# Kernel tuning notes

Measured on AMD Instinct MI355X. Metric: run time of the kernel, lower is better.

Reference implementation:

```python
import jax, jax.numpy as jnp
import numpy as np

N_EMBED = 1024
EMBED_DIM = 64
DECAY = 0.99
EPS = 1e-05


def setup_inputs() -> dict:
    key = jax.random.key(0)
    k1, k2 = jax.random.split(key)
    z_e = jax.random.normal(k1, (16, 4096, EMBED_DIM), dtype=jnp.float32)
    # torch init: uniform_(-1/n_embed, 1/n_embed)
    embed = (jax.random.uniform(k2, (N_EMBED, EMBED_DIM), dtype=jnp.float32) * 2.0 - 1.0) / N_EMBED
    cluster_size = jnp.zeros((N_EMBED,), dtype=jnp.float32)
    embed_avg = embed.copy()
    return {"z_e": z_e, "embed": embed, "cluster_size": cluster_size, "embed_avg": embed_avg}


def reference(z_e, embed, cluster_size, embed_avg):
    B, N, E = z_e.shape
    flat = z_e.reshape(-1, E)  # [T, E], T = B*N
    dist = (jnp.sum(flat * flat, axis=1, keepdims=True)
            - 2.0 * flat @ embed.T
            + jnp.sum(embed * embed, axis=1)[None, :])  # [T, K]
    embed_ind = jnp.argmin(dist, axis=1)  # argmax(-dist)
    z_q = embed[embed_ind].reshape(B, N, E)

    # training-mode EMA statistics (scatter-add == one-hot matmul, but memory-efficient)
    onehot_sum = jnp.zeros((N_EMBED,), flat.dtype).at[embed_ind].add(1.0)
    embed_sum = jnp.zeros((N_EMBED, E), flat.dtype).at[embed_ind].add(flat)
    new_cluster_size = DECAY * cluster_size + (1.0 - DECAY) * onehot_sum
    new_embed_avg = DECAY * embed_avg + (1.0 - DECAY) * embed_sum
    n = jnp.sum(new_cluster_size)
    cs = (new_cluster_size + EPS) / (n + N_EMBED * EPS) * n
    new_embed = new_embed_avg / cs[:, None]

    diff = jnp.mean((jax.lax.stop_gradient(z_q) - z_e) ** 2)
    z_q_st = z_e + jax.lax.stop_gradient(z_q - z_e)  # straight-through
    return (z_q_st, diff, embed_ind.reshape(B, N), new_embed, new_cluster_size, new_embed_avg)
```

## Files before the change

### kernel.cpp

```cpp
#include <hip/hip_runtime.h>
#include <math.h>

#define T_TOK 65536
#define K_CODE 1024
#define E_DIM 64
#define DECAYF 0.99f
#define EPSF 1e-5f

#define TT 256
#define QCAP 4096
#define HACC 1.3e-3f

typedef short short8 __attribute__((ext_vector_type(8)));
typedef float f32x16 __attribute__((ext_vector_type(16)));

__device__ __forceinline__ float mul_nf(float a, float b) {
#pragma clang fp contract(off)
    return a * b;
}
__device__ __forceinline__ float add_nf(float a, float b) {
#pragma clang fp contract(off)
    return a + b;
}
__device__ __forceinline__ float sub_nf(float a, float b) {
#pragma clang fp contract(off)
    return a - b;
}

__device__ __forceinline__ float np_sq_row(const float* xrow) {
    const float4* xp = reinterpret_cast<const float4*>(xrow);
    float r[8];
#pragma unroll
    for (int g = 0; g < 8; ++g) {
        float4 va = xp[2 * g], vb = xp[2 * g + 1];
        float e[8] = {va.x, va.y, va.z, va.w, vb.x, vb.y, vb.z, vb.w};
#pragma unroll
        for (int j = 0; j < 8; ++j) {
            if (g == 0) r[j] = mul_nf(e[j], e[j]);
            else        r[j] = add_nf(r[j], mul_nf(e[j], e[j]));
        }
    }
    float s01 = add_nf(r[0], r[1]);
    float s23 = add_nf(r[2], r[3]);
    float s45 = add_nf(r[4], r[5]);
    float s67 = add_nf(r[6], r[7]);
    return add_nf(add_nf(s01, s23), add_nf(s45, s67));
}

__device__ __forceinline__ unsigned f2bf_rne(float f) {
    unsigned u = __float_as_uint(f);
    u += 0x7FFFu + ((u >> 16) & 1u);
    return (u >> 16);
}

__device__ __forceinline__ void exact_key(int t0, int tl, int code, float wn,
                                          const float* __restrict__ z_e,
                                          const float* __restrict__ embed,
                                          const float* xn_s,
                                          unsigned long long* key_s) {
    const float4* xp = reinterpret_cast<const float4*>(z_e + (size_t)(t0 + tl) * E_DIM);
    const float4* wp = reinterpret_cast<const float4*>(embed + (size_t)code * E_DIM);
    float d = 0.f;
#pragma unroll
    for (int m = 0; m < 16; ++m) {
        float4 x4 = xp[m];
        float4 w4 = wp[m];
        d = __builtin_fmaf(x4.x, w4.x, d);
        d = __builtin_fmaf(x4.y, w4.y, d);
        d = __builtin_fmaf(x4.z, w4.z, d);
        d = __builtin_fmaf(x4.w, w4.w, d);
    }
    float dist = add_nf(sub_nf(xn_s[tl], d + d), wn);
    unsigned b = __float_as_uint(dist);
    unsigned mk = (b & 0x80000000u) ? ~b : (b | 0x80000000u);
    atomicMin(key_s + tl, ((unsigned long long)mk << 32) | (unsigned)code);
}


__global__ __launch_bounds__(512) void dist_kernel(const float* __restrict__ z_e,
                                                   const float* __restrict__ embed,
                                                   float* __restrict__ out_zq,
                                                   float* __restrict__ out_ind,
                                                   float* __restrict__ diff_acc,
                                                   float* __restrict__ esum_rep,
                                                   float* __restrict__ onehot_rep,
                                                   int rep_mask) {
    __shared__ unsigned short Ws[K_CODE * E_DIM];
    __shared__ float wn_s[K_CODE];
    __shared__ float xn_s[TT];
    __shared__ unsigned long long key_s[TT];
    __shared__ unsigned q_s[QCAP];
    __shared__ int bi_s[TT];
    __shared__ int qc_s;

    int tid = threadIdx.x;
    int lane = tid & 63;
    int wave = tid >> 6;
    int g = lane >> 5;
    int t0 = blockIdx.x * TT;

    if (tid == 0) qc_s = 0;
    if (tid < TT) {
        key_s[tid] = ~0ull;
        xn_s[tid] = np_sq_row(z_e + (size_t)(t0 + tid) * E_DIM);
    }

#pragma unroll
    for (int rr = 0; rr < 2; ++rr) {
        int row = tid + rr * 512;
        const float4* wp = reinterpret_cast<const float4*>(embed + (size_t)row * E_DIM);
        uint4* WsQ = reinterpret_cast<uint4*>(Ws);
        float r8[8];
#pragma unroll
        for (int gq = 0; gq < 8; ++gq) {
            float4 va = wp[2 * gq], vb = wp[2 * gq + 1];
            float e[8] = {va.x, va.y, va.z, va.w, vb.x, vb.y, vb.z, vb.w};
#pragma unroll
            for (int j = 0; j < 8; ++j) {
                if (gq == 0) r8[j] = mul_nf(e[j], e[j]);
                else         r8[j] = add_nf(r8[j], mul_nf(e[j], e[j]));
            }
            unsigned p0 = f2bf_rne(e[0]) | (f2bf_rne(e[1]) << 16);
            unsigned p1 = f2bf_rne(e[2]) | (f2bf_rne(e[3]) << 16);
            unsigned p2 = f2bf_rne(e[4]) | (f2bf_rne(e[5]) << 16);
            unsigned p3 = f2bf_rne(e[6]) | (f2bf_rne(e[7]) << 16);
            WsQ[row * 8 + (gq ^ (row & 7))] = make_uint4(p0, p1, p2, p3);
        }
        float s01 = add_nf(r8[0], r8[1]);
        float s23 = add_nf(r8[2], r8[3]);
        float s45 = add_nf(r8[4], r8[5]);
        float s67 = add_nf(r8[6], r8[7]);
        wn_s[row] = add_nf(add_nf(s01, s23), add_nf(s45, s67));
    }

    int arow = wave * 32 + (lane & 31);
    const float* xrow = z_e + (size_t)(t0 + arow) * E_DIM;
    short8 afr[4];
#pragma unroll
    for (int kc = 0; kc < 4; ++kc) {
        int base = kc * 16 + g * 8;
        float4 a = *reinterpret_cast<const float4*>(xrow + base);
        float4 b = *reinterpret_cast<const float4*>(xrow + base + 4);
        afr[kc][0] = (short)f2bf_rne(a.x);
        afr[kc][1] = (short)f2bf_rne(a.y);
        afr[kc][2] = (short)f2bf_rne(a.z);
        afr[kc][3] = (short)f2bf_rne(a.w);
        afr[kc][4] = (short)f2bf_rne(b.x);
        afr[kc][5] = (short)f2bf_rne(b.y);
        afr[kc][6] = (short)f2bf_rne(b.z);
        afr[kc][7] = (short)f2bf_rne(b.w);
    }

    __syncthreads();

    float maxr[16], thr[16];
#pragma unroll
    for (int r = 0; r < 16; ++r) maxr[r] = -INFINITY;

#pragma unroll 4
    for (int tile = 0; tile < 32; ++tile) {
        int code = tile * 32 + (lane & 31);
        f32x16 acc;
#pragma unroll
        for (int i = 0; i < 16; ++i) acc[i] = 0.f;
#pragma unroll
        for (int kc = 0; kc < 4; ++kc) {
            int ps = (2 * kc + g) ^ (code & 7);
            short8 bfr = *reinterpret_cast<const short8*>(&Ws[code * E_DIM + ps * 8]);
            acc = __builtin_amdgcn_mfma_f32_32x32x16_bf16(afr[kc], bfr, acc, 0, 0, 0);
        }
#pragma unroll
        for (int r = 0; r < 16; ++r) maxr[r] = fmaxf(maxr[r], acc[r]);
        if ((tile & 3) == 0) {
#pragma unroll
            for (int off = 1; off < 32; off <<= 1) {
#pragma unroll
                for (int r = 0; r < 16; ++r)
                    maxr[r] = fmaxf(maxr[r], __shfl_xor(maxr[r], off, 64));
            }
#pragma unroll
            for (int r = 0; r < 16; ++r) thr[r] = maxr[r] - HACC;
        }
        float tmax = -INFINITY;
#pragma unroll
        for (int r = 0; r < 16; ++r) tmax = fmaxf(tmax, acc[r] - thr[r]);
        if (tmax >= 0.f) {
#pragma unroll
            for (int r = 0; r < 16; ++r) {
                if (acc[r] >= thr[r]) {
                    int row = (r & 3) + 8 * (r >> 2) + 4 * g;
                    int tl = wave * 32 + row;
                    int slot = atomicAdd(&qc_s, 1);
                    if (slot < QCAP)
                        q_s[slot] = ((unsigned)tl << 10) | (unsigned)code;
                    else
                        exact_key(t0, tl, code, wn_s[code], z_e, embed, xn_s, key_s);
                }
            }
        }
    }
    __syncthreads();

    int qn = qc_s;
    if (qn > QCAP) qn = QCAP;
    for (int e = tid; e < qn; e += 512) {
        unsigned q = q_s[e];
        int tl = (int)(q >> 10);
        int code = (int)(q & 1023u);
        exact_key(t0, tl, code, wn_s[code], z_e, embed, xn_s, key_s);
    }
    __syncthreads();

    if (tid < TT) {
        int bi = (int)(unsigned)(key_s[tid] & 1023ull);
        bi_s[tid] = bi;
        out_ind[t0 + tid] = (float)bi;
    }
    __syncthreads();

    int rep = blockIdx.x & rep_mask;
    float* esum = esum_rep + (size_t)rep * (K_CODE * E_DIM);
    float* onehot = onehot_rep + (size_t)rep * K_CODE;

    float ds = 0.f;
#pragma unroll 4
    for (int it = 0; it < 32; ++it) {
        int tl = wave * 32 + it;
        int bi = bi_s[tl];
        float xv = z_e[(size_t)(t0 + tl) * E_DIM + lane];
        float wv = embed[(size_t)bi * E_DIM + lane];
        float rr = sub_nf(wv, xv);
        out_zq[(size_t)(t0 + tl) * E_DIM + lane] = add_nf(xv, rr);
        ds = __builtin_fmaf(rr, rr, ds);
        atomicAdd(&esum[(size_t)bi * E_DIM + lane], xv);
        if (lane == 0) atomicAdd(&onehot[bi], 1.0f);
    }
#pragma unroll
    for (int o = 32; o > 0; o >>= 1) ds += __shfl_down(ds, o, 64);
    if (lane == 0) atomicAdd(diff_acc, ds);
}

__global__ __launch_bounds__(256) void finalize_kernel(const float* __restrict__ cluster_size,
                                                       const float* __restrict__ onehot_rep,
                                                       const float* __restrict__ ws_diff,
                                                       const float* __restrict__ embed_avg,
                                                       const float* __restrict__ esum_rep,
                                                       float* __restrict__ out_diff,
                                                       float* __restrict__ out_ncs,
                                                       float* __restrict__ out_ne,
                                                       float* __restrict__ out_nea,
                                                       int nrep) {
    __shared__ float ncs_s[K_CODE];
    __shared__ float red[K_CODE];
    int tid = threadIdx.x;

#pragma unroll
    for (int i = 0; i < 4; ++i) {
        int k = tid + 256 * i;
        float oh = 0.f;
        for (int r = 0; r < nrep; ++r) oh += onehot_rep[(size_t)r * K_CODE + k];
        float ncs = DECAYF * cluster_size[k] + (1.0f - DECAYF) * oh;
        ncs_s[k] = ncs;
        red[k] = ncs;
    }
    __syncthreads();
    for (int s = 512; s > 0; s >>= 1) {
        for (int idx = tid; idx < s; idx += 256) red[idx] += red[idx + s];
        __syncthreads();
    }
    float n = red[0];

    if (blockIdx.x == 0) {
#pragma unroll
        for (int i = 0; i < 4; ++i) {
            int k = tid + 256 * i;
            out_ncs[k] = ncs_s[k];
        }
        if (tid == 0) out_diff[0] = ws_diff[0] * (1.0f / 4194304.0f);
    }

    int k = blockIdx.x * 16 + (tid >> 4);
    int c = tid & 15;
    float ncs = ncs_s[k];
    float cs = (ncs + EPSF) / (n + (float)K_CODE * EPSF) * n;

    size_t off = (size_t)k * E_DIM + (size_t)c * 4;
    float4 s4 = make_float4(0.f, 0.f, 0.f, 0.f);
    for (int r = 0; r < nrep; ++r) {
        float4 v = *reinterpret_cast<const float4*>(esum_rep + (size_t)r * (K_CODE * E_DIM) + off);
        s4.x += v.x; s4.y += v.y; s4.z += v.z; s4.w += v.w;
    }
    float4 a = *reinterpret_cast<const float4*>(embed_avg + off);
    float4 nea, ne;
    nea.x = DECAYF * a.x + (1.0f - DECAYF) * s4.x;
    nea.y = DECAYF * a.y + (1.0f - DECAYF) * s4.y;
    nea.z = DECAYF * a.z + (1.0f - DECAYF) * s4.z;
    nea.w = DECAYF * a.w + (1.0f - DECAYF) * s4.w;
    ne.x = nea.x / cs; ne.y = nea.y / cs; ne.z = nea.z / cs; ne.w = nea.w / cs;
    *reinterpret_cast<float4*>(out_nea + off) = nea;
    *reinterpret_cast<float4*>(out_ne + off) = ne;
}

extern "C" void kernel_launch(void* const* d_in, const int* in_sizes, int n_in,
                              void* d_out, int out_size, void* d_ws, size_t ws_size,
                              hipStream_t stream) {
    const float* z_e = (const float*)d_in[0];
    const float* embed = (const float*)d_in[1];
    const float* cluster_size = (const float*)d_in[2];
    const float* embed_avg = (const float*)d_in[3];

    float* out = (float*)d_out;
    float* o_zq = out;
    float* o_diff = out + 4194304;
    float* o_ind = out + 4194305;
    float* o_ne = out + 4194305 + 65536;
    float* o_ncs = o_ne + 65536;
    float* o_nea = o_ncs + 1024;

    float* ws = (float*)d_ws;
    float* ws_diff = ws + 0;
    float* ws_onehot = ws + 16;

    int nrep = 1;
    while (nrep < 8 &&
           (size_t)(8208 + (size_t)(2 * nrep) * 65536) * sizeof(float) <= ws_size)
        nrep *= 2;

    float* ws_esum = ws + 8208;

    hipMemsetAsync(ws, 0, (size_t)(8208 + (size_t)nrep * 65536) * sizeof(float), stream);

    dist_kernel<<<T_TOK / TT, 512, 0, stream>>>(z_e, embed, o_zq, o_ind, ws_diff,
                                                ws_esum, ws_onehot, nrep - 1);
    finalize_kernel<<<64, 256, 0, stream>>>(cluster_size, ws_onehot, ws_diff, embed_avg,
                                            ws_esum, o_diff, o_ncs, o_ne, o_nea, nrep);
}
```

Measured before the change: 224.0 us.

## Use two-pass exact-max screening with 4-way MFMA batching per iteration

```diff
diff --git a/kernel.cpp b/kernel.cpp
--- a/kernel.cpp
+++ b/kernel.cpp
@@ -8,7 +8,7 @@
 #define EPSF 1e-5f
 
 #define TT 256
-#define QCAP 4096
+#define QCAP 2048
 #define HACC 1.3e-3f
 
 typedef short short8 __attribute__((ext_vector_type(8)));
@@ -153,48 +153,88 @@
 
     __syncthreads();
 
-    float maxr[16], thr[16];
+    float maxr[16];
 #pragma unroll
     for (int r = 0; r < 16; ++r) maxr[r] = -INFINITY;
 
-#pragma unroll 4
-    for (int tile = 0; tile < 32; ++tile) {
-        int code = tile * 32 + (lane & 31);
-        f32x16 acc;
-#pragma unroll
-        for (int i = 0; i < 16; ++i) acc[i] = 0.f;
+#pragma unroll 1
+    for (int tq = 0; tq < 8; ++tq) {
+        int c0 = tq * 128 + (lane & 31);
+        f32x16 A0, A1, A2, A3;
+#pragma unroll
+        for (int i = 0; i < 16; ++i) { A0[i] = 0.f; A1[i] = 0.f; A2[i] = 0.f; A3[i] = 0.f; }
 #pragma unroll
         for (int kc = 0; kc < 4; ++kc) {
-            int ps = (2 * kc + g) ^ (code & 7);
-            short8 bfr = *reinterpret_cast<const short8*>(&Ws[code * E_DIM + ps * 8]);
-            acc = __builtin_amdgcn_mfma_f32_32x32x16_bf16(afr[kc], bfr, acc, 0, 0, 0);
-        }
-#pragma unroll
-        for (int r = 0; r < 16; ++r) maxr[r] = fmaxf(maxr[r], acc[r]);
-        if ((tile & 3) == 0) {
-#pragma unroll
-            for (int off = 1; off < 32; off <<= 1) {
-#pragma unroll
-                for (int r = 0; r < 16; ++r)
-                    maxr[r] = fmaxf(maxr[r], __shfl_xor(maxr[r], off, 64));
-            }
-#pragma unroll
-            for (int r = 0; r < 16; ++r) thr[r] = maxr[r] - HACC;
+            int ps = (2 * kc + g) ^ (c0 & 7);
+            const unsigned short* wsb = &Ws[c0 * E_DIM + ps * 8];
+            short8 b0 = *reinterpret_cast<const short8*>(wsb);
+            short8 b1 = *reinterpret_cast<const short8*>(wsb + 32 * E_DIM);
+            short8 b2 = *reinterpret_cast<const short8*>(wsb + 64 * E_DIM);
+            short8 b3 = *reinterpret_cast<const short8*>(wsb + 96 * E_DIM);
+            A0 = __builtin_amdgcn_mfma_f32_32x32x16_bf16(afr[kc], b0, A0, 0, 0, 0);
+            A1 = __builtin_amdgcn_mfma_f32_32x32x16_bf16(afr[kc], b1, A1, 0, 0, 0);
+            A2 = __builtin_amdgcn_mfma_f32_32x32x16_bf16(afr[kc], b2, A2, 0, 0, 0);
+            A3 = __builtin_amdgcn_mfma_f32_32x32x16_bf16(afr[kc], b3, A3, 0, 0, 0);
+        }
+#pragma unroll
+        for (int r = 0; r < 16; ++r) {
+            float m01 = fmaxf(A0[r], A1[r]);
+            float m23 = fmaxf(A2[r], A3[r]);
+            maxr[r] = fmaxf(maxr[r], fmaxf(m01, m23));
+        }
+    }
+
+#pragma unroll
+    for (int off = 1; off < 32; off <<= 1) {
+#pragma unroll
+        for (int r = 0; r < 16; ++r)
+            maxr[r] = fmaxf(maxr[r], __shfl_xor(maxr[r], off, 64));
+    }
+#pragma unroll
+    for (int r = 0; r < 16; ++r) maxr[r] -= HACC;
+
+#pragma unroll 1
+    for (int tq = 0; tq < 8; ++tq) {
+        int c0 = tq * 128 + (lane & 31);
+        f32x16 A0, A1, A2, A3;
+#pragma unroll
+        for (int i = 0; i < 16; ++i) { A0[i] = 0.f; A1[i] = 0.f; A2[i] = 0.f; A3[i] = 0.f; }
+#pragma unroll
+        for (int kc = 0; kc < 4; ++kc) {
+            int ps = (2 * kc + g) ^ (c0 & 7);
+            const unsigned short* wsb = &Ws[c0 * E_DIM + ps * 8];
+            short8 b0 = *reinterpret_cast<const short8*>(wsb);
+            short8 b1 = *reinterpret_cast<const short8*>(wsb + 32 * E_DIM);
+            short8 b2 = *reinterpret_cast<const short8*>(wsb + 64 * E_DIM);
+            short8 b3 = *reinterpret_cast<const short8*>(wsb + 96 * E_DIM);
+            A0 = __builtin_amdgcn_mfma_f32_32x32x16_bf16(afr[kc], b0, A0, 0, 0, 0);
+            A1 = __builtin_amdgcn_mfma_f32_32x32x16_bf16(afr[kc], b1, A1, 0, 0, 0);
+            A2 = __builtin_amdgcn_mfma_f32_32x32x16_bf16(afr[kc], b2, A2, 0, 0, 0);
+            A3 = __builtin_amdgcn_mfma_f32_32x32x16_bf16(afr[kc], b3, A3, 0, 0, 0);
         }
         float tmax = -INFINITY;
 #pragma unroll
-        for (int r = 0; r < 16; ++r) tmax = fmaxf(tmax, acc[r] - thr[r]);
+        for (int r = 0; r < 16; ++r) {
+            float m01 = fmaxf(A0[r], A1[r]);
+            float m23 = fmaxf(A2[r], A3[r]);
+            tmax = fmaxf(tmax, fmaxf(m01, m23) - maxr[r]);
+        }
         if (tmax >= 0.f) {
 #pragma unroll
             for (int r = 0; r < 16; ++r) {
-                if (acc[r] >= thr[r]) {
-                    int row = (r & 3) + 8 * (r >> 2) + 4 * g;
-                    int tl = wave * 32 + row;
-                    int slot = atomicAdd(&qc_s, 1);
-                    if (slot < QCAP)
-                        q_s[slot] = ((unsigned)tl << 10) | (unsigned)code;
-                    else
-                        exact_key(t0, tl, code, wn_s[code], z_e, embed, xn_s, key_s);
+                float av[4] = {A0[r], A1[r], A2[r], A3[r]};
+#pragma unroll
+                for (int t = 0; t < 4; ++t) {
+                    if (av[t] >= maxr[r]) {
+                        int row = (r & 3) + 8 * (r >> 2) + 4 * g;
+                        int tl = wave * 32 + row;
+                        int code = c0 + 32 * t;
+                        int slot = atomicAdd(&qc_s, 1);
+                        if (slot < QCAP)
+                            q_s[slot] = ((unsigned)tl << 10) | (unsigned)code;
+                        else
+                            exact_key(t0, tl, code, wn_s[code], z_e, embed, xn_s, key_s);
+                    }
                 }
             }
         }
```

Measured after the change: 184.2 us. -17.8%, faster.
